# Kernel optimization log

Measured on AMD Instinct MI355X. Metric: run time of the kernel, lower is better.

Reference implementation:

```python
import jax, jax.numpy as jnp
import numpy as np

BN_EPS = 1e-5


def setup_inputs() -> dict:
    key = jax.random.key(0)
    k1, k2 = jax.random.split(key)
    bs, planes, h, w = 16, 64, 256, 256
    x = jax.random.normal(k1, (bs, planes, h, w), dtype=jnp.float32)
    # kaiming_normal_ on (planes, h, h): fan_in = h*h, std = sqrt(2/fan_in)
    std = np.sqrt(2.0 / (h * h)).astype(np.float32)
    weights = jax.random.normal(k2, (planes, h, h), dtype=jnp.float32) * std
    gamma = jnp.ones((planes,), dtype=jnp.float32)
    beta = jnp.zeros((planes,), dtype=jnp.float32)
    return {"x": x, "weights": weights, "gamma": gamma, "beta": beta}


def reference(x, weights, gamma, beta):
    bs, planes, h, w = x.shape
    xf = x.reshape(bs * planes, h, w)
    # batched Gram matrix: [bs*planes, h, h]
    g = jnp.einsum('nij,nkj->nik', xf, xf)
    g = jnp.triu(g)                              # keep upper triangle (incl. diag)
    g = g.reshape(bs, planes, h, h) * weights[None]  # per-plane elementwise weight
    # BatchNorm2d (training mode): biased batch stats over (N, H, W) per channel
    mean = jnp.mean(g, axis=(0, 2, 3), keepdims=True)
    var = jnp.mean(jnp.square(g - mean), axis=(0, 2, 3), keepdims=True)
    g_hat = (g - mean) * jax.lax.rsqrt(var + BN_EPS)
    out = g_hat * gamma[None, :, None, None] + beta[None, :, None, None]
    return out
```

## Files before the change

### kernel.cpp

```cpp
#include <hip/hip_runtime.h>

#define HD 256
#define NCH 64
#define NB 16
#define NPLANE (NB * NCH)
#define NPC (NB * HD * HD)
#define PLANE_ELEMS (HD * HD)

typedef __attribute__((ext_vector_type(4))) float f32x4;
typedef __attribute__((ext_vector_type(8))) short s16x8;
typedef __attribute__((ext_vector_type(4))) short s16x4;

__device__ __forceinline__ short f2bf(float f) {
    unsigned u = __float_as_uint(f);
    u += 0x7FFFu + ((u >> 16) & 1u);
    return (short)(u >> 16);
}
__device__ __forceinline__ float bf2f(short s) {
    return __uint_as_float(((unsigned)(unsigned short)s) << 16);
}

__device__ __forceinline__ s16x8 ldfrag(const short* B, int row, int q) {
    return *(const s16x8*)&B[row * 64 + ((q ^ (row & 7)) << 3)];
}

__global__ __launch_bounds__(512, 2) void gram_kernel(
    const float* __restrict__ x, const float* __restrict__ w,
    short* __restrict__ raw, float* __restrict__ stats)
{
    const int n    = blockIdx.x;
    const int c    = n & (NCH - 1);
    const int tid  = threadIdx.x;
    const int wid  = tid >> 6;
    const int lane = tid & 63;
    const int waveM = wid >> 2;
    const int waveN = wid & 3;
    const int lrow  = lane & 15;
    const int qlane = lane >> 4;

    __shared__ short As[2][16384];
    __shared__ float redS[8], redQ[8];

    const float* xp = x + (size_t)n * PLANE_ELEMS;
    const int rs = tid >> 3;
    const int qs = tid & 7;

    f32x4 accA[4][4], accB[4][2];
    #pragma unroll
    for (int i = 0; i < 4; ++i) {
        #pragma unroll
        for (int j = 0; j < 4; ++j) accA[i][j] = (f32x4){0.f, 0.f, 0.f, 0.f};
        accB[i][0] = (f32x4){0.f, 0.f, 0.f, 0.f};
        accB[i][1] = (f32x4){0.f, 0.f, 0.f, 0.f};
    }

    f32x4 lr[4][2];

    #pragma unroll
    for (int j = 0; j < 4; ++j) {
        const float* p = xp + (size_t)(j * 64 + rs) * HD + qs * 8;
        lr[j][0] = *(const f32x4*)p;
        lr[j][1] = *(const f32x4*)(p + 4);
    }
    #pragma unroll
    for (int j = 0; j < 4; ++j) {
        const int row = j * 64 + rs;
        s16x8 o = { f2bf(lr[j][0].x), f2bf(lr[j][0].y), f2bf(lr[j][0].z), f2bf(lr[j][0].w),
                    f2bf(lr[j][1].x), f2bf(lr[j][1].y), f2bf(lr[j][1].z), f2bf(lr[j][1].w) };
        *(s16x8*)&As[0][row * 64 + ((qs ^ (row & 7)) << 3)] = o;
    }

    #pragma unroll
    for (int kc = 0; kc < 4; ++kc) {
        __syncthreads();
        if (kc < 3) {
            #pragma unroll
            for (int j = 0; j < 4; ++j) {
                const float* p = xp + (size_t)(j * 64 + rs) * HD + (kc + 1) * 64 + qs * 8;
                lr[j][0] = *(const f32x4*)p;
                lr[j][1] = *(const f32x4*)(p + 4);
            }
        }
        const short* B = As[kc & 1];
        #pragma unroll
        for (int kk = 0; kk < 2; ++kk) {
            const int q = kk * 4 + qlane;
            s16x8 a0[4], b0[4];
            #pragma unroll
            for (int mi = 0; mi < 4; ++mi)
                a0[mi] = ldfrag(B, waveM * 64 + mi * 16 + lrow, q);
            #pragma unroll
            for (int ni = 0; ni < 4; ++ni)
                b0[ni] = ldfrag(B, waveN * 64 + ni * 16 + lrow, q);
            #pragma unroll
            for (int mi = 0; mi < 4; ++mi)
                #pragma unroll
                for (int ni = 0; ni < 4; ++ni)
                    accA[mi][ni] = __builtin_amdgcn_mfma_f32_16x16x32_bf16(
                        a0[mi], b0[ni], accA[mi][ni], 0, 0, 0);
            s16x8 a1[4], b1[2];
            #pragma unroll
            for (int mi = 0; mi < 4; ++mi)
                a1[mi] = ldfrag(B, 128 + waveM * 64 + mi * 16 + lrow, q);
            #pragma unroll
            for (int ni = 0; ni < 2; ++ni)
                b1[ni] = ldfrag(B, 128 + waveN * 32 + ni * 16 + lrow, q);
            #pragma unroll
            for (int mi = 0; mi < 4; ++mi)
                #pragma unroll
                for (int ni = 0; ni < 2; ++ni)
                    accB[mi][ni] = __builtin_amdgcn_mfma_f32_16x16x32_bf16(
                        a1[mi], b1[ni], accB[mi][ni], 0, 0, 0);
        }
        if (kc < 3) {
            #pragma unroll
            for (int j = 0; j < 4; ++j) {
                const int row = j * 64 + rs;
                s16x8 o = { f2bf(lr[j][0].x), f2bf(lr[j][0].y), f2bf(lr[j][0].z), f2bf(lr[j][0].w),
                            f2bf(lr[j][1].x), f2bf(lr[j][1].y), f2bf(lr[j][1].z), f2bf(lr[j][1].w) };
                *(s16x8*)&As[(kc + 1) & 1][row * 64 + ((qs ^ (row & 7)) << 3)] = o;
            }
        }
    }

    const float* wp = w + (size_t)c * PLANE_ELEMS;
    short* rp = raw + (size_t)n * PLANE_ELEMS;
    float lsum = 0.f, lsq = 0.f;
    const int row0 = qlane * 4;
    const int col0 = lrow;
    #pragma unroll
    for (int mi = 0; mi < 4; ++mi) {
        #pragma unroll
        for (int ni = 0; ni < 4; ++ni) {
            const int gk = waveN * 64 + ni * 16 + col0;
            #pragma unroll
            for (int r = 0; r < 4; ++r) {
                const int gi = waveM * 64 + mi * 16 + row0 + r;
                float v = accA[mi][ni][r];
                float val = (gk >= gi) ? v * wp[gi * HD + gk] : 0.f;
                lsum += val;
                lsq  += val * val;
                rp[gi * HD + gk] = f2bf(val);
            }
        }
        #pragma unroll
        for (int ni = 0; ni < 2; ++ni) {
            const int gk = 128 + waveN * 32 + ni * 16 + col0;
            #pragma unroll
            for (int r = 0; r < 4; ++r) {
                const int gi = 128 + waveM * 64 + mi * 16 + row0 + r;
                float v = accB[mi][ni][r];
                float val = (gk >= gi) ? v * wp[gi * HD + gk] : 0.f;
                lsum += val;
                lsq  += val * val;
                rp[gi * HD + gk] = f2bf(val);
            }
        }
    }

    #pragma unroll
    for (int off = 32; off > 0; off >>= 1) {
        lsum += __shfl_down(lsum, off);
        lsq  += __shfl_down(lsq, off);
    }
    if (lane == 0) { redS[wid] = lsum; redQ[wid] = lsq; }
    __syncthreads();
    if (tid == 0) {
        float s = 0.f, s2 = 0.f;
        #pragma unroll
        for (int i = 0; i < 8; ++i) { s += redS[i]; s2 += redQ[i]; }
        atomicAdd(&stats[2 * c],     s);
        atomicAdd(&stats[2 * c + 1], s2);
    }
}

__global__ __launch_bounds__(256) void bn_kernel(
    const float* __restrict__ gamma, const float* __restrict__ beta,
    float* __restrict__ out, const float* __restrict__ stats,
    const short* __restrict__ raw)
{
    const int n   = blockIdx.x;
    const int seg = blockIdx.y;
    const int tid = threadIdx.x;
    const int c   = n & (NCH - 1);

    float s  = stats[2 * c];
    float sq = stats[2 * c + 1];
    float mean = s * (1.0f / (float)NPC);
    float var  = sq * (1.0f / (float)NPC) - mean * mean;
    float rstd = rsqrtf(var + 1e-5f);
    float scale = rstd * gamma[c];
    float shift = beta[c] - mean * scale;

    const short* rp = raw + (size_t)n * PLANE_ELEMS;
    float* op = out + (size_t)n * PLANE_ELEMS;
    f32x4 cv = {shift, shift, shift, shift};

    #pragma unroll
    for (int k = 0; k < 2; ++k) {
        const int idx8 = seg * 512 + k * 256 + tid;
        const int r  = idx8 >> 5;
        const int c8 = idx8 & 31;
        const bool cst = (r < 128) ? ((c8 * 8 + 7) < r)
                                   : (c8 < 16 || (((c8 - 16) * 8 + 7) < (r - 128)));
        float* o = &op[(size_t)idx8 * 8];
        if (cst) {
            *(f32x4*)o       = cv;
            *(f32x4*)(o + 4) = cv;
        } else {
            s16x8 v = *(const s16x8*)&rp[(size_t)idx8 * 8];
            f32x4 lo = { bf2f(v[0]) * scale + shift, bf2f(v[1]) * scale + shift,
                         bf2f(v[2]) * scale + shift, bf2f(v[3]) * scale + shift };
            f32x4 hi = { bf2f(v[4]) * scale + shift, bf2f(v[5]) * scale + shift,
                         bf2f(v[6]) * scale + shift, bf2f(v[7]) * scale + shift };
            *(f32x4*)o       = lo;
            *(f32x4*)(o + 4) = hi;
        }
    }
}

template <int PASS>
__global__ __launch_bounds__(256) void gram_bn_fb(
    const float* __restrict__ x, const float* __restrict__ w,
    const float* __restrict__ gamma, const float* __restrict__ beta,
    float* __restrict__ out, float* __restrict__ stats)
{
    const int tile = blockIdx.x;
    const int b    = blockIdx.y;
    const int c    = blockIdx.z;
    const int n    = b * NCH + c;
    const int tid  = threadIdx.x;

    float mean = 0.f, rstd = 0.f, gm = 0.f, bt = 0.f;
    if (PASS == 1) {
        float s  = stats[2*c];
        float sq = stats[2*c+1];
        mean = s * (1.0f / (float)NPC);
        float var = sq * (1.0f / (float)NPC) - mean * mean;
        rstd = rsqrtf(var + 1e-5f);
        gm = gamma[c]; bt = beta[c];
    }
    if (PASS == 1 && tile == 3) {
        float v = (0.f - mean) * rstd * gm + bt;
        f32x4 vv = {v, v, v, v};
        float* op = out + (size_t)n * PLANE_ELEMS;
        for (int it = 0; it < 16; ++it) {
            int t  = it * 256 + tid;
            int r  = t >> 5;
            int c4 = (t & 31) * 4;
            *(f32x4*)&op[(size_t)(128 + r) * HD + c4] = vv;
        }
        return;
    }
    int ti, tk;
    if      (tile == 0) { ti = 0; tk = 0; }
    else if (tile == 1) { ti = 0; tk = 1; }
    else                { ti = 1; tk = 1; }
    const float* xp = x + (size_t)n * PLANE_ELEMS;
    __shared__ short As[128 * 40];
    __shared__ short Bs[128 * 40];
    __shared__ float red[512];
    const int wid   = tid >> 6;
    const int lane  = tid & 63;
    const int waveM = wid >> 1, waveN = wid & 1;
    const int lrow  = lane & 15;
    const int lkk   = (lane >> 4) * 8;
    f32x4 acc[4][4];
    for (int i = 0; i < 4; ++i)
        for (int j = 0; j < 4; ++j)
            acc[i][j] = (f32x4){0.f, 0.f, 0.f, 0.f};
    const int rr = tid >> 3;
    const int cc = (tid & 7) * 4;
    for (int kb = 0; kb < 8; ++kb) {
        for (int it = 0; it < 4; ++it) {
            int r = rr + it * 32;
            f32x4 av = *(const f32x4*)&xp[(size_t)(ti*128 + r) * HD + kb*32 + cc];
            f32x4 bv = *(const f32x4*)&xp[(size_t)(tk*128 + r) * HD + kb*32 + cc];
            s16x4 a4 = { f2bf(av.x), f2bf(av.y), f2bf(av.z), f2bf(av.w) };
            s16x4 b4 = { f2bf(bv.x), f2bf(bv.y), f2bf(bv.z), f2bf(bv.w) };
            *(s16x4*)&As[r*40 + cc] = a4;
            *(s16x4*)&Bs[r*40 + cc] = b4;
        }
        __syncthreads();
        s16x8 af[4], bfr[4];
        for (int mi = 0; mi < 4; ++mi)
            af[mi]  = *(s16x8*)&As[(waveM*64 + mi*16 + lrow)*40 + lkk];
        for (int ni = 0; ni < 4; ++ni)
            bfr[ni] = *(s16x8*)&Bs[(waveN*64 + ni*16 + lrow)*40 + lkk];
        for (int mi = 0; mi < 4; ++mi)
            for (int ni = 0; ni < 4; ++ni)
                acc[mi][ni] = __builtin_amdgcn_mfma_f32_16x16x32_bf16(
                    af[mi], bfr[ni], acc[mi][ni], 0, 0, 0);
        __syncthreads();
    }
    float lsum = 0.f, lsq = 0.f;
    const int row0 = (lane >> 4) * 4;
    const int col0 = lane & 15;
    for (int mi = 0; mi < 4; ++mi) {
        for (int ni = 0; ni < 4; ++ni) {
            int gk = tk*128 + waveN*64 + ni*16 + col0;
            for (int r = 0; r < 4; ++r) {
                int gi = ti*128 + waveM*64 + mi*16 + row0 + r;
                float v = acc[mi][ni][r];
                float val = (gk >= gi)
                    ? v * w[(size_t)c * PLANE_ELEMS + (size_t)gi * HD + gk]
                    : 0.f;
                if (PASS == 0) { lsum += val; lsq += val * val; }
                else out[(size_t)n * PLANE_ELEMS + (size_t)gi * HD + gk] =
                        (val - mean) * rstd * gm + bt;
            }
        }
    }
    if (PASS == 0) {
        red[tid] = lsum; red[256 + tid] = lsq;
        __syncthreads();
        for (int s = 128; s > 0; s >>= 1) {
            if (tid < s) { red[tid] += red[tid+s]; red[256+tid] += red[256+tid+s]; }
            __syncthreads();
        }
        if (tid == 0) {
            atomicAdd(&stats[2*c],     red[0]);
            atomicAdd(&stats[2*c + 1], red[256]);
        }
    }
}

extern "C" void kernel_launch(void* const* d_in, const int* in_sizes, int n_in,
                              void* d_out, int out_size, void* d_ws, size_t ws_size,
                              hipStream_t stream) {
    const float* x     = (const float*)d_in[0];
    const float* w     = (const float*)d_in[1];
    const float* gamma = (const float*)d_in[2];
    const float* beta  = (const float*)d_in[3];
    float* out   = (float*)d_out;
    float* stats = (float*)d_ws;

    hipMemsetAsync(d_ws, 0, 128 * sizeof(float), stream);

    const size_t raw_bytes = (size_t)NPLANE * PLANE_ELEMS * sizeof(short);
    if (ws_size >= 1024 + raw_bytes) {
        short* raw = (short*)((char*)d_ws + 1024);
        gram_kernel<<<dim3(NPLANE), dim3(512), 0, stream>>>(x, w, raw, stats);
        bn_kernel<<<dim3(NPLANE, 16), dim3(256), 0, stream>>>(gamma, beta, out, stats, raw);
    } else {
        gram_bn_fb<0><<<dim3(3, NB, NCH), dim3(256), 0, stream>>>(x, w, gamma, beta, out, stats);
        gram_bn_fb<1><<<dim3(4, NB, NCH), dim3(256), 0, stream>>>(x, w, gamma, beta, out, stats);
    }
}
```

Before: 614.2 us.

## Split per-plane Gram into three 128x128 tile blocks for more parallelism

The Gram kernel now launches one block per 128x128 upper-triangular quadrant (3 per plane) instead of one block per plane computing all three quadrants. Each block keeps half the accumulators, and launch bounds are raised to allow 4 blocks per CU. Diagonal tiles load only one row-slab and reuse it for both operands; the off-diagonal tile loads two slabs into separate LDS buffers. The goal is better occupancy and load balance across CUs. The cost is that each plane's input rows are read from global memory twice instead of once.

```diff
diff --git a/kernel.cpp b/kernel.cpp
--- a/kernel.cpp
+++ b/kernel.cpp
@@ -20,54 +20,70 @@
     return __uint_as_float(((unsigned)(unsigned short)s) << 16);
 }
 
-__device__ __forceinline__ s16x8 ldfrag(const short* B, int row, int q) {
+__device__ __forceinline__ s16x8 ldfrag64(const short* B, int row, int q) {
     return *(const s16x8*)&B[row * 64 + ((q ^ (row & 7)) << 3)];
 }
 
-__global__ __launch_bounds__(512, 2) void gram_kernel(
+__global__ __launch_bounds__(512, 4) void gram_kernel(
     const float* __restrict__ x, const float* __restrict__ w,
     short* __restrict__ raw, float* __restrict__ stats)
 {
-    const int n    = blockIdx.x;
-    const int c    = n & (NCH - 1);
-    const int tid  = threadIdx.x;
-    const int wid  = tid >> 6;
-    const int lane = tid & 63;
+    const int tile = blockIdx.x;
+    const int ti = (tile == 2) ? 1 : 0;
+    const int tk = (tile == 0) ? 0 : 1;
+    const bool diag = (ti == tk);
+    const int b = blockIdx.y;
+    const int c = blockIdx.z;
+    const int n = b * NCH + c;
+    const int tid = threadIdx.x;
+    const int wid = tid >> 6, lane = tid & 63;
     const int waveM = wid >> 2;
     const int waveN = wid & 3;
-    const int lrow  = lane & 15;
+    const int lrow = lane & 15;
     const int qlane = lane >> 4;
 
-    __shared__ short As[2][16384];
+    __shared__ short As[2][8192];
+    __shared__ short Bs[2][8192];
     __shared__ float redS[8], redQ[8];
 
-    const float* xp = x + (size_t)n * PLANE_ELEMS;
+    const float* xpA = x + (size_t)n * PLANE_ELEMS + (size_t)(ti * 128) * HD;
+    const float* xpB = x + (size_t)n * PLANE_ELEMS + (size_t)(tk * 128) * HD;
+
     const int rs = tid >> 3;
     const int qs = tid & 7;
 
-    f32x4 accA[4][4], accB[4][2];
+    f32x4 acc[4][2];
     #pragma unroll
     for (int i = 0; i < 4; ++i) {
-        #pragma unroll
-        for (int j = 0; j < 4; ++j) accA[i][j] = (f32x4){0.f, 0.f, 0.f, 0.f};
-        accB[i][0] = (f32x4){0.f, 0.f, 0.f, 0.f};
-        accB[i][1] = (f32x4){0.f, 0.f, 0.f, 0.f};
-    }
-
-    f32x4 lr[4][2];
-
-    #pragma unroll
-    for (int j = 0; j < 4; ++j) {
-        const float* p = xp + (size_t)(j * 64 + rs) * HD + qs * 8;
-        lr[j][0] = *(const f32x4*)p;
-        lr[j][1] = *(const f32x4*)(p + 4);
-    }
-    #pragma unroll
-    for (int j = 0; j < 4; ++j) {
+        acc[i][0] = (f32x4){0.f, 0.f, 0.f, 0.f};
+        acc[i][1] = (f32x4){0.f, 0.f, 0.f, 0.f};
+    }
+
+    f32x4 lA[2][2], lB[2][2];
+
+    #pragma unroll
+    for (int j = 0; j < 2; ++j) {
+        const float* pA = xpA + (size_t)(j * 64 + rs) * HD + qs * 8;
+        lA[j][0] = *(const f32x4*)pA;
+        lA[j][1] = *(const f32x4*)(pA + 4);
+        if (!diag) {
+            const float* pB = xpB + (size_t)(j * 64 + rs) * HD + qs * 8;
+            lB[j][0] = *(const f32x4*)pB;
+            lB[j][1] = *(const f32x4*)(pB + 4);
+        }
+    }
+    #pragma unroll
+    for (int j = 0; j < 2; ++j) {
         const int row = j * 64 + rs;
-        s16x8 o = { f2bf(lr[j][0].x), f2bf(lr[j][0].y), f2bf(lr[j][0].z), f2bf(lr[j][0].w),
-                    f2bf(lr[j][1].x), f2bf(lr[j][1].y), f2bf(lr[j][1].z), f2bf(lr[j][1].w) };
-        *(s16x8*)&As[0][row * 64 + ((qs ^ (row & 7)) << 3)] = o;
+        const int off = row * 64 + ((qs ^ (row & 7)) << 3);
+        s16x8 oa = { f2bf(lA[j][0].x), f2bf(lA[j][0].y), f2bf(lA[j][0].z), f2bf(lA[j][0].w),
+                     f2bf(lA[j][1].x), f2bf(lA[j][1].y), f2bf(lA[j][1].z), f2bf(lA[j][1].w) };
+        *(s16x8*)&As[0][off] = oa;
+        if (!diag) {
+            s16x8 ob = { f2bf(lB[j][0].x), f2bf(lB[j][0].y), f2bf(lB[j][0].z), f2bf(lB[j][0].w),
+                         f2bf(lB[j][1].x), f2bf(lB[j][1].y), f2bf(lB[j][1].z), f2bf(lB[j][1].w) };
+            *(s16x8*)&Bs[0][off] = ob;
+        }
     }
 
     #pragma unroll
@@ -75,50 +91,49 @@
         __syncthreads();
         if (kc < 3) {
             #pragma unroll
-            for (int j = 0; j < 4; ++j) {
-                const float* p = xp + (size_t)(j * 64 + rs) * HD + (kc + 1) * 64 + qs * 8;
-                lr[j][0] = *(const f32x4*)p;
-                lr[j][1] = *(const f32x4*)(p + 4);
+            for (int j = 0; j < 2; ++j) {
+                const float* pA = xpA + (size_t)(j * 64 + rs) * HD + (kc + 1) * 64 + qs * 8;
+                lA[j][0] = *(const f32x4*)pA;
+                lA[j][1] = *(const f32x4*)(pA + 4);
+                if (!diag) {
+                    const float* pB = xpB + (size_t)(j * 64 + rs) * HD + (kc + 1) * 64 + qs * 8;
+                    lB[j][0] = *(const f32x4*)pB;
+                    lB[j][1] = *(const f32x4*)(pB + 4);
+                }
             }
         }
-        const short* B = As[kc & 1];
+        const short* Ab = As[kc & 1];
+        const short* Bb = diag ? Ab : Bs[kc & 1];
         #pragma unroll
         for (int kk = 0; kk < 2; ++kk) {
             const int q = kk * 4 + qlane;
-            s16x8 a0[4], b0[4];
+            s16x8 af[4], bf[2];
             #pragma unroll
             for (int mi = 0; mi < 4; ++mi)
-                a0[mi] = ldfrag(B, waveM * 64 + mi * 16 + lrow, q);
-            #pragma unroll
-            for (int ni = 0; ni < 4; ++ni)
-                b0[ni] = ldfrag(B, waveN * 64 + ni * 16 + lrow, q);
-            #pragma unroll
-            for (int mi = 0; mi < 4; ++mi)
-                #pragma unroll
-                for (int ni = 0; ni < 4; ++ni)
-                    accA[mi][ni] = __builtin_amdgcn_mfma_f32_16x16x32_bf16(
-                        a0[mi], b0[ni], accA[mi][ni], 0, 0, 0);
-            s16x8 a1[4], b1[2];
-            #pragma unroll
-            for (int mi = 0; mi < 4; ++mi)
-                a1[mi] = ldfrag(B, 128 + waveM * 64 + mi * 16 + lrow, q);
+                af[mi] = ldfrag64(Ab, waveM * 64 + mi * 16 + lrow, q);
             #pragma unroll
             for (int ni = 0; ni < 2; ++ni)
-                b1[ni] = ldfrag(B, 128 + waveN * 32 + ni * 16 + lrow, q);
+                bf[ni] = ldfrag64(Bb, waveN * 32 + ni * 16 + lrow, q);
             #pragma unroll
             for (int mi = 0; mi < 4; ++mi)
                 #pragma unroll
                 for (int ni = 0; ni < 2; ++ni)
-                    accB[mi][ni] = __builtin_amdgcn_mfma_f32_16x16x32_bf16(
-                        a1[mi], b1[ni], accB[mi][ni], 0, 0, 0);
+                    acc[mi][ni] = __builtin_amdgcn_mfma_f32_16x16x32_bf16(
+                        af[mi], bf[ni], acc[mi][ni], 0, 0, 0);
         }
         if (kc < 3) {
             #pragma unroll
-            for (int j = 0; j < 4; ++j) {
+            for (int j = 0; j < 2; ++j) {
                 const int row = j * 64 + rs;
-                s16x8 o = { f2bf(lr[j][0].x), f2bf(lr[j][0].y), f2bf(lr[j][0].z), f2bf(lr[j][0].w),
-                            f2bf(lr[j][1].x), f2bf(lr[j][1].y), f2bf(lr[j][1].z), f2bf(lr[j][1].w) };
-                *(s16x8*)&As[(kc + 1) & 1][row * 64 + ((qs ^ (row & 7)) << 3)] = o;
+                const int off = row * 64 + ((qs ^ (row & 7)) << 3);
+                s16x8 oa = { f2bf(lA[j][0].x), f2bf(lA[j][0].y), f2bf(lA[j][0].z), f2bf(lA[j][0].w),
+                             f2bf(lA[j][1].x), f2bf(lA[j][1].y), f2bf(lA[j][1].z), f2bf(lA[j][1].w) };
+                *(s16x8*)&As[(kc + 1) & 1][off] = oa;
+                if (!diag) {
+                    s16x8 ob = { f2bf(lB[j][0].x), f2bf(lB[j][0].y), f2bf(lB[j][0].z), f2bf(lB[j][0].w),
+                                 f2bf(lB[j][1].x), f2bf(lB[j][1].y), f2bf(lB[j][1].z), f2bf(lB[j][1].w) };
+                    *(s16x8*)&Bs[(kc + 1) & 1][off] = ob;
+                }
             }
         }
     }
@@ -131,26 +146,14 @@
     #pragma unroll
     for (int mi = 0; mi < 4; ++mi) {
         #pragma unroll
-        for (int ni = 0; ni < 4; ++ni) {
-            const int gk = waveN * 64 + ni * 16 + col0;
+        for (int ni = 0; ni < 2; ++ni) {
+            const int gk = tk * 128 + waveN * 32 + ni * 16 + col0;
             #pragma unroll
             for (int r = 0; r < 4; ++r) {
-                const int gi = waveM * 64 + mi * 16 + row0 + r;
-                float v = accA[mi][ni][r];
-                float val = (gk >= gi) ? v * wp[gi * HD + gk] : 0.f;
-                lsum += val;
-                lsq  += val * val;
-                rp[gi * HD + gk] = f2bf(val);
-            }
-        }
-        #pragma unroll
-        for (int ni = 0; ni < 2; ++ni) {
-            const int gk = 128 + waveN * 32 + ni * 16 + col0;
-            #pragma unroll
-            for (int r = 0; r < 4; ++r) {
-                const int gi = 128 + waveM * 64 + mi * 16 + row0 + r;
-                float v = accB[mi][ni][r];
-                float val = (gk >= gi) ? v * wp[gi * HD + gk] : 0.f;
+                const int gi = ti * 128 + waveM * 64 + mi * 16 + row0 + r;
+                const bool keep = diag ? (gk >= gi) : true;
+                float v = acc[mi][ni][r];
+                float val = keep ? v * wp[gi * HD + gk] : 0.f;
                 lsum += val;
                 lsq  += val * val;
                 rp[gi * HD + gk] = f2bf(val);
@@ -340,7 +343,7 @@
     const size_t raw_bytes = (size_t)NPLANE * PLANE_ELEMS * sizeof(short);
     if (ws_size >= 1024 + raw_bytes) {
         short* raw = (short*)((char*)d_ws + 1024);
-        gram_kernel<<<dim3(NPLANE), dim3(512), 0, stream>>>(x, w, raw, stats);
+        gram_kernel<<<dim3(3, NB, NCH), dim3(512), 0, stream>>>(x, w, raw, stats);
         bn_kernel<<<dim3(NPLANE, 16), dim3(256), 0, stream>>>(gamma, beta, out, stats, raw);
     } else {
         gram_bn_fb<0><<<dim3(3, NB, NCH), dim3(256), 0, stream>>>(x, w, gamma, beta, out, stats);
```

Result: faster. 599.6 us (-2.4%).
